# Kernel optimization log

Measured on AMD Instinct MI355X. Metric: run time of the kernel, lower is better.

The kernel has to match this reference:

```python
import jax, jax.numpy as jnp
import numpy as np

N = 50000      # nodes
E = 600000     # edges
H = 128        # hidden_features (= in_features)
ED = 16        # edge_attr_dim
B = 256        # number of graphs in batch
L = 5          # num_layers
OUT = 128      # out_features


def _xavier(key, shape):
    fan_in, fan_out = shape
    a = float(np.sqrt(6.0 / (fan_in + fan_out)))
    return jax.random.uniform(key, shape, jnp.float32, -a, a)


def setup_inputs() -> dict:
    key = jax.random.key(0)
    ks = jax.random.split(key, 32)
    x = jax.random.normal(ks[0], (N, H), jnp.float32)
    edge_index = jax.random.randint(ks[1], (2, E), 0, N, jnp.int32)
    edge_attr = jax.random.normal(ks[2], (E, ED), jnp.float32)
    batch = jnp.sort(jax.random.randint(ks[3], (N,), 0, B, jnp.int32))
    # per-layer parameters, stacked along leading L axis (in=hidden so uniform)
    node_W = jnp.stack([_xavier(jax.random.fold_in(ks[4], i), (H, H)) for i in range(L)])
    edge_W = jnp.stack([_xavier(jax.random.fold_in(ks[5], i), (ED, H)) for i in range(L)])
    mlp1_W = jnp.stack([_xavier(jax.random.fold_in(ks[6], i), (H, H)) for i in range(L)])
    mlp2_W = jnp.stack([_xavier(jax.random.fold_in(ks[7], i), (H, H)) for i in range(L)])
    zb = jnp.zeros((L, H), jnp.float32)
    # virtual-node update MLP (shared across layers) and final classifier
    vn_w0 = _xavier(ks[8], (H, H)); vn_b0 = jnp.zeros((H,), jnp.float32)
    vn_w1 = _xavier(ks[9], (H, H)); vn_b1 = jnp.zeros((H,), jnp.float32)
    fc_W = _xavier(ks[10], (H, OUT)); fc_b = jnp.zeros((OUT,), jnp.float32)
    vn_init = jnp.zeros((1, H), jnp.float32)  # embedding initialized to 0
    return {
        "x": x, "edge_attr": edge_attr,
        "node_W": node_W, "node_b": zb, "edge_W": edge_W, "edge_b": zb,
        "mlp1_W": mlp1_W, "mlp1_b": zb, "mlp2_W": mlp2_W, "mlp2_b": zb,
        "vn_w0": vn_w0, "vn_b0": vn_b0, "vn_w1": vn_w1, "vn_b1": vn_b1,
        "fc_W": fc_W, "fc_b": fc_b, "vn_init": vn_init,
        "edge_index": edge_index, "batch": batch,
    }


def reference(x, edge_attr, node_W, node_b, edge_W, edge_b, mlp1_W, mlp1_b,
              mlp2_W, mlp2_b, vn_w0, vn_b0, vn_w1, vn_b1, fc_W, fc_b,
              vn_init, edge_index, batch):
    src, dst = edge_index[0], edge_index[1]
    # per-graph node counts for mean pooling (guard against empty graphs)
    counts = jnp.maximum(
        jax.ops.segment_sum(jnp.ones((N, 1), x.dtype), batch, num_segments=B), 1.0)
    vn = jnp.broadcast_to(vn_init, (B, H))  # weight.repeat(batch_size, 1)

    def layer(carry, p):
        xc, vn = carry
        nW, nb, eW, eb, m1W, m1b, m2W, m2b = p
        h = xc @ nW + nb + vn[batch]              # node encode + VN broadcast
        ea = edge_attr @ eW + eb                   # edge encode [E,H]
        msg = h[src] + ea                          # gather + add
        agg = jax.ops.segment_sum(msg, dst, num_segments=N)  # scatter-add
        out = jax.nn.relu(agg @ m1W + m1b) @ m2W + m2b        # layer MLP
        xn = jax.nn.relu(out)
        pooled = jax.ops.segment_sum(xn, batch, num_segments=B) / counts
        vn2 = vn + jax.nn.relu(jax.nn.relu(pooled @ vn_w0 + vn_b0) @ vn_w1 + vn_b1)
        return (xn, vn2), None

    (xf, _), _ = jax.lax.scan(
        layer, (x, vn),
        (node_W, node_b, edge_W, edge_b, mlp1_W, mlp1_b, mlp2_W, mlp2_b))
    pooled = jax.ops.segment_sum(xf, batch, num_segments=B) / counts
    return pooled @ fc_W + fc_b
```

## Files before the change

### kernel.cpp

```cpp
#include <hip/hip_runtime.h>

#define NN 50000
#define EE 600000
#define HH 128
#define EDD 16
#define BB 256
#define LL 5
#define NN16 (NN * 16)
#define NSHADOW 8
#define GN 782

typedef float f32x4 __attribute__((ext_vector_type(4)));
typedef _Float16 f16x4 __attribute__((ext_vector_type(4)));
typedef _Float16 f16x8 __attribute__((ext_vector_type(8)));

__global__ __launch_bounds__(256) void wprep_all_k(
    const float* __restrict__ W0, const float* __restrict__ W1, const float* __restrict__ W2,
    _Float16* __restrict__ H0, _Float16* __restrict__ L0,
    _Float16* __restrict__ H1, _Float16* __restrict__ L1,
    _Float16* __restrict__ H2, _Float16* __restrict__ L2,
    const float* __restrict__ eW, const float* __restrict__ eb, const float* __restrict__ nb,
    _Float16* __restrict__ BXh, _Float16* __restrict__ BXl)
{
    int idx = blockIdx.x * 256 + threadIdx.x;
    if (idx < 3 * 81920) {
        int seg = idx / 81920, r = idx - seg * 81920;
        const float* W = (seg == 0) ? W0 : (seg == 1) ? W1 : W2;
        _Float16* Wh = (seg == 0) ? H0 : (seg == 1) ? H1 : H2;
        _Float16* Wl = (seg == 0) ? L0 : (seg == 1) ? L1 : L2;
        int mat = r >> 14;
        int rr = r & 16383;
        int j = rr & 7, lane = (rr >> 3) & 63, ks = (rr >> 9) & 3, ntw = (rr >> 11) & 7;
        int lm = lane & 15, quad = lane >> 4;
        int n = (ntw >> 1) * 32 + (ntw & 1) * 16 + lm;
        int k = ks * 32 + quad * 8 + j;
        float w = W[(mat << 14) + (k << 7) + n];
        _Float16 h = (_Float16)w;
        Wh[r] = h;
        Wl[r] = (_Float16)(w - (float)h);
    } else {
        int i2 = idx - 3 * 81920;
        if (i2 >= 5 * 8192) return;
        int j = i2 & 7, lane = (i2 >> 3) & 63, ks = (i2 >> 9) & 1, ntw = (i2 >> 10) & 7, l = i2 >> 13;
        int lm = lane & 15, quad = lane >> 4;
        int n = (ntw >> 1) * 32 + (ntw & 1) * 16 + lm;
        int k = ks * 32 + quad * 8 + j;
        float v = 0.f;
        if (k < 16) v = eW[((size_t)l * 16 + k) * 128 + n];
        else if (k < 32) v = eW[((size_t)l * 16 + (k - 16)) * 128 + n];
        else if (k == 32) v = eb[l * 128 + n] + nb[l * 128 + n];
        _Float16 h = (_Float16)v;
        BXh[i2] = h;
        BXl[i2] = (_Float16)(v - (float)h);
    }
}

__global__ __launch_bounds__(256) void misc_k(const float* __restrict__ x, _Float16* __restrict__ X0,
    const float* __restrict__ vninit, float* __restrict__ vn, _Float16* __restrict__ vnB,
    float* __restrict__ pooled8)
{
    int i = blockIdx.x * 256 + threadIdx.x;
    if (i < NN * 32) {
        float4 v = ((const float4*)x)[i];
        f16x4 o;
        o[0] = (_Float16)v.x; o[1] = (_Float16)v.y; o[2] = (_Float16)v.z; o[3] = (_Float16)v.w;
        ((f16x4*)X0)[i] = o;
    } else {
        int k = i - NN * 32;
        if (k < NSHADOW * BB * HH) pooled8[k] = 0.f;
        if (k < BB * HH) { vn[k] = vninit[k & 127]; vnB[k] = (_Float16)0; }
    }
}

__device__ __forceinline__ void mfma_stage16(
    const _Float16* __restrict__ As,
    const _Float16* __restrict__ Wh, const _Float16* __restrict__ Wl,
    int wn, int lm, int quad, int lane, f32x4 acc[4][2])
{
    f16x8 Bh[2][4], Bl[2][4];
#pragma unroll
    for (int nt = 0; nt < 2; ++nt)
#pragma unroll
        for (int ks = 0; ks < 4; ++ks) {
            int fi = ((((wn * 2 + nt) * 4) + ks) * 64 + lane) * 8;
            Bh[nt][ks] = *(const f16x8*)(Wh + fi);
            Bl[nt][ks] = *(const f16x8*)(Wl + fi);
        }
#pragma unroll
    for (int ks = 0; ks < 4; ++ks) {
        f16x8 a[4];
#pragma unroll
        for (int mt = 0; mt < 4; ++mt) {
            int off = (mt * 16 + lm) * 136 + ks * 32 + quad * 8;
            a[mt] = *(const f16x8*)(As + off);
        }
#pragma unroll
        for (int mt = 0; mt < 4; ++mt)
#pragma unroll
            for (int nt = 0; nt < 2; ++nt) {
                acc[mt][nt] = __builtin_amdgcn_mfma_f32_16x16x32_f16(a[mt], Bh[nt][ks], acc[mt][nt], 0, 0, 0);
                acc[mt][nt] = __builtin_amdgcn_mfma_f32_16x16x32_f16(a[mt], Bl[nt][ks], acc[mt][nt], 0, 0, 0);
            }
    }
}

__device__ __forceinline__ void store_f16(const _Float16* __restrict__ Fo,
    _Float16* __restrict__ out, int M, int brow, int tid)
{
    const int r = tid >> 2, cg = tid & 3;
    const int grow = brow + r;
    if (grow >= M) return;
    const f16x8* src = (const f16x8*)(Fo + r * 136 + cg * 32);
    f16x8* dst = (f16x8*)(out + (size_t)grow * 128 + cg * 32);
#pragma unroll
    for (int i = 0; i < 4; ++i) dst[i] = src[i];
}

__global__ __launch_bounds__(256) void layer_k(
    const _Float16* __restrict__ Xin,
    const _Float16* __restrict__ Afix,
    const _Float16* __restrict__ Cfrag, const _Float16* __restrict__ vnB, int usevn,
    const int* __restrict__ rowstart, const int2* __restrict__ csr,
    const _Float16* __restrict__ WNh, const _Float16* __restrict__ WNl,
    const _Float16* __restrict__ BXh, const _Float16* __restrict__ BXl,
    const _Float16* __restrict__ W1h, const _Float16* __restrict__ W1l, const float* __restrict__ b1,
    const _Float16* __restrict__ W2h, const _Float16* __restrict__ W2l, const float* __restrict__ b2,
    _Float16* __restrict__ Xout, float* __restrict__ pooled8,
    const int* __restrict__ batch, int M)
{
    __shared__ __align__(16) _Float16 bufA[64 * 136];
    __shared__ __align__(16) _Float16 bufB[64 * 136];
    const int tid = threadIdx.x, brow = blockIdx.x * 64;

    {
        const int r = tid >> 2, cg = tid & 3;
        const int grow = brow + r;
        _Float16* p = bufB + r * 72 + cg * 16;
        if (grow < M) {
            const f16x8* s = (const f16x8*)(Afix + (size_t)grow * 64 + cg * 16);
            ((f16x8*)p)[0] = s[0]; ((f16x8*)p)[1] = s[1];
        } else {
            f16x8 z = (f16x8)(_Float16)0;
            ((f16x8*)p)[0] = z; ((f16x8*)p)[1] = z;
        }
    }

    {
        const int wv = tid >> 6, grp = (tid >> 4) & 3, li = tid & 15;
        const f16x8* X8 = (const f16x8*)Xin;
        for (int j = 0; j < 4; ++j) {
            int rnode = wv * 16 + grp * 4 + j;
            int node = brow + rnode;
            f16x8 o = (f16x8)(_Float16)0;
            if (node < M) {
                int s = rowstart[node], e = rowstart[node + 1];
                float ax[8];
#pragma unroll
                for (int k = 0; k < 8; ++k) ax[k] = 0.f;
                int p = s;
                for (; p + 4 <= e; p += 4) {
                    int s0 = csr[p].x, s1 = csr[p + 1].x, s2 = csr[p + 2].x, s3 = csr[p + 3].x;
                    f16x8 x0 = X8[(size_t)s0 * 16 + li];
                    f16x8 x1 = X8[(size_t)s1 * 16 + li];
                    f16x8 x2 = X8[(size_t)s2 * 16 + li];
                    f16x8 x3 = X8[(size_t)s3 * 16 + li];
#pragma unroll
                    for (int k = 0; k < 8; ++k)
                        ax[k] += ((float)x0[k] + (float)x1[k]) + ((float)x2[k] + (float)x3[k]);
                }
                for (; p < e; ++p) {
                    f16x8 x0 = X8[(size_t)csr[p].x * 16 + li];
#pragma unroll
                    for (int k = 0; k < 8; ++k) ax[k] += (float)x0[k];
                }
#pragma unroll
                for (int k = 0; k < 8; ++k) o[k] = (_Float16)ax[k];
            }
            *(f16x8*)(bufA + rnode * 136 + li * 8) = o;
        }
    }
    __syncthreads();

    const int lane = tid & 63, wn = tid >> 6, lm = lane & 15, quad = lane >> 4;
    const int colb = wn * 32 + lm;

    f32x4 acc[4][2];
#pragma unroll
    for (int mt = 0; mt < 4; ++mt) { acc[mt][0] = (f32x4)(0.f); acc[mt][1] = (f32x4)(0.f); }

    mfma_stage16(bufA, WNh, WNl, wn, lm, quad, lane, acc);

#pragma unroll
    for (int ksf = 0; ksf < 2; ++ksf) {
        f16x8 Bh[2], Bl[2];
#pragma unroll
        for (int nt = 0; nt < 2; ++nt) {
            int fi = (((wn * 2 + nt) * 2 + ksf) * 64 + lane) * 8;
            Bh[nt] = *(const f16x8*)(BXh + fi);
            Bl[nt] = *(const f16x8*)(BXl + fi);
        }
#pragma unroll
        for (int mt = 0; mt < 4; ++mt) {
            f16x8 a = *(const f16x8*)(bufB + (mt * 16 + lm) * 72 + ksf * 32 + quad * 8);
#pragma unroll
            for (int nt = 0; nt < 2; ++nt) {
                acc[mt][nt] = __builtin_amdgcn_mfma_f32_16x16x32_f16(a, Bh[nt], acc[mt][nt], 0, 0, 0);
                acc[mt][nt] = __builtin_amdgcn_mfma_f32_16x16x32_f16(a, Bl[nt], acc[mt][nt], 0, 0, 0);
            }
        }
    }

    if (usevn) {
        const _Float16* Cb = Cfrag + (size_t)blockIdx.x * 16384;
#pragma unroll
        for (int ks = 0; ks < 8; ++ks) {
            f16x8 bv[2];
#pragma unroll
            for (int nt = 0; nt < 2; ++nt)
                bv[nt] = *(const f16x8*)(vnB + (((ks * 8 + (wn * 2 + nt)) * 64 + lane) * 8));
#pragma unroll
            for (int mt = 0; mt < 4; ++mt) {
                f16x8 av = *(const f16x8*)(Cb + (((mt * 8 + ks) * 64 + lane) * 8));
                acc[mt][0] = __builtin_amdgcn_mfma_f32_16x16x32_f16(av, bv[0], acc[mt][0], 0, 0, 0);
                acc[mt][1] = __builtin_amdgcn_mfma_f32_16x16x32_f16(av, bv[1], acc[mt][1], 0, 0, 0);
            }
        }
    }
    __syncthreads();

#pragma unroll
    for (int mt = 0; mt < 4; ++mt) {
#pragma unroll
        for (int r = 0; r < 4; ++r) {
            int trow = mt * 16 + quad * 4 + r;
            bufA[trow * 136 + colb]      = (_Float16)acc[mt][0][r];
            bufA[trow * 136 + colb + 16] = (_Float16)acc[mt][1][r];
        }
    }
    __syncthreads();

#pragma unroll
    for (int mt = 0; mt < 4; ++mt) { acc[mt][0] = (f32x4)(0.f); acc[mt][1] = (f32x4)(0.f); }
    mfma_stage16(bufA, W1h, W1l, wn, lm, quad, lane, acc);
    {
        const float c0 = b1[colb], c1 = b1[colb + 16];
#pragma unroll
        for (int mt = 0; mt < 4; ++mt) {
#pragma unroll
            for (int r = 0; r < 4; ++r) {
                int trow = mt * 16 + quad * 4 + r;
                bufB[trow * 136 + colb]      = (_Float16)fmaxf(acc[mt][0][r] + c0, 0.f);
                bufB[trow * 136 + colb + 16] = (_Float16)fmaxf(acc[mt][1][r] + c1, 0.f);
            }
        }
    }
    __syncthreads();

#pragma unroll
    for (int mt = 0; mt < 4; ++mt) { acc[mt][0] = (f32x4)(0.f); acc[mt][1] = (f32x4)(0.f); }
    mfma_stage16(bufB, W2h, W2l, wn, lm, quad, lane, acc);
    {
        const float d0 = b2[colb], d1 = b2[colb + 16];
#pragma unroll
        for (int mt = 0; mt < 4; ++mt) {
#pragma unroll
            for (int r = 0; r < 4; ++r) {
                int trow = mt * 16 + quad * 4 + r;
                bufA[trow * 136 + colb]      = (_Float16)fmaxf(acc[mt][0][r] + d0, 0.f);
                bufA[trow * 136 + colb + 16] = (_Float16)fmaxf(acc[mt][1][r] + d1, 0.f);
            }
        }
    }
    __syncthreads();
    store_f16(bufA, Xout, M, brow, tid);

    {
        float* pooled = pooled8 + (size_t)(blockIdx.x & (NSHADOW - 1)) * (BB * HH);
        const int c = tid & 127, half = tid >> 7;
        const int row0 = half * 32;
        float sum = 0.f;
        int curg = -1;
        for (int r2 = 0; r2 < 32; ++r2) {
            int grow = brow + row0 + r2;
            if (grow >= M) break;
            int g = batch[grow];
            if (g != curg) {
                if (curg >= 0) atomicAdd(&pooled[curg * 128 + c], sum);
                curg = g; sum = 0.f;
            }
            sum += (float)bufA[(row0 + r2) * 136 + c];
        }
        if (curg >= 0) atomicAdd(&pooled[curg * 128 + c], sum);
    }
}

__global__ __launch_bounds__(256) void aggfix_k(
    const float* __restrict__ eattr, const int* __restrict__ rowstart,
    const int2* __restrict__ csr, _Float16* __restrict__ Afix, int n)
{
    const int lane = threadIdx.x & 15;
    const int node = blockIdx.x * 16 + (threadIdx.x >> 4);
    if (node >= n) return;
    const int s = rowstart[node], e = rowstart[node + 1];
    float acc = 0.f;
    for (int p = s; p < e; ++p)
        acc += eattr[(size_t)csr[p].y * 16 + lane];
    _Float16 hi = (_Float16)acc;
    _Float16 lo = (_Float16)(acc - (float)hi);
    _Float16* A = Afix + (size_t)node * 64;
    A[lane] = hi;
    A[16 + lane] = lo;
    A[32 + lane] = (lane == 0) ? (_Float16)(float)(e - s) : (_Float16)0;
    A[48 + lane] = (_Float16)0;
}

__global__ void histboth_k(const int* __restrict__ dstv, const int* __restrict__ srcv,
                           const int* __restrict__ batch,
                           int* __restrict__ degp, unsigned int* __restrict__ Cpack)
{
    int i = blockIdx.x * 256 + threadIdx.x;
    if (i >= EE) return;
    int d = dstv[i];
    atomicAdd(&degp[(blockIdx.x & 3) * NN16 + (d << 4)], 1);
    int g = batch[srcv[i]];
    int blk = d >> 6, rib = d & 63, mt = rib >> 4, lm = rib & 15;
    int ks = g >> 5, quad = (g >> 3) & 3, j = g & 7;
    size_t e = (size_t)blk * 16384 + (size_t)(((mt * 8 + ks) * 64) + quad * 16 + lm) * 8 + j;
    atomicAdd(&Cpack[e >> 1], 1u << ((e & 1) * 16));
}

__global__ __launch_bounds__(256) void ccvt_k(unsigned int* __restrict__ Cpack)
{
    int i = blockIdx.x * 256 + threadIdx.x;
    if (i >= GN * 16384 / 2) return;
    unsigned int v = Cpack[i];
    _Float16 lo = (_Float16)(float)(v & 0xffffu);
    _Float16 hi = (_Float16)(float)(v >> 16);
    unsigned short lu = __builtin_bit_cast(unsigned short, lo);
    unsigned short hu = __builtin_bit_cast(unsigned short, hi);
    Cpack[i] = (unsigned int)lu | ((unsigned int)hu << 16);
}

__global__ __launch_bounds__(128) void vn_update_k(
    float* __restrict__ pooled8, const int* __restrict__ gstart,
    const float* __restrict__ W0, const float* __restrict__ b0,
    const float* __restrict__ W1, const float* __restrict__ b1,
    float* __restrict__ vn, _Float16* __restrict__ vnB)
{
    __shared__ float p[128], q[128];
    const int g = blockIdx.x, t = threadIdx.x;
    float cnt = (float)(gstart[g + 1] - gstart[g]);
    if (cnt < 1.f) cnt = 1.f;
    float sum = 0.f;
#pragma unroll
    for (int s = 0; s < NSHADOW; ++s) {
        float* slot = pooled8 + (size_t)s * (BB * HH) + g * 128 + t;
        sum += *slot;
        *slot = 0.f;
    }
    p[t] = sum / cnt;
    __syncthreads();
    float a0 = b0[t];
    for (int k = 0; k < 128; ++k) a0 = fmaf(p[k], W0[k * 128 + t], a0);
    q[t] = fmaxf(a0, 0.f);
    __syncthreads();
    float a1 = b1[t];
    for (int k = 0; k < 128; ++k) a1 = fmaf(q[k], W1[k * 128 + t], a1);
    float nv = vn[g * 128 + t] + fmaxf(a1, 0.f);
    vn[g * 128 + t] = nv;
    {
        int ks = g >> 5, quad = (g >> 3) & 3, j = g & 7;
        int tt = ((t >> 5) << 1) | ((t >> 4) & 1);
        int lanev = quad * 16 + (t & 15);
        vnB[((ks * 8 + tt) * 64 + lanev) * 8 + j] = (_Float16)nv;
    }
}

__global__ __launch_bounds__(128) void fc_k(
    const float* __restrict__ pooled8, const int* __restrict__ gstart,
    const float* __restrict__ W, const float* __restrict__ b,
    float* __restrict__ out)
{
    __shared__ float p[128];
    const int g = blockIdx.x, t = threadIdx.x;
    float cnt = (float)(gstart[g + 1] - gstart[g]);
    if (cnt < 1.f) cnt = 1.f;
    float sum = 0.f;
#pragma unroll
    for (int s = 0; s < NSHADOW; ++s)
        sum += pooled8[(size_t)s * (BB * HH) + g * 128 + t];
    p[t] = sum / cnt;
    __syncthreads();
    float acc = b[t];
    for (int k = 0; k < 128; ++k) acc = fmaf(p[k], W[k * 128 + t], acc);
    out[g * 128 + t] = acc;
}

__global__ void scan_deg_k(const int* __restrict__ degp, int n, int* __restrict__ out, int* __restrict__ bsum)
{
    __shared__ int s[256];
    int gid = blockIdx.x * 256 + threadIdx.x;
    int v = 0;
    if (gid < n) {
        int o = gid << 4;
        v = degp[o] + degp[NN16 + o] + degp[2 * NN16 + o] + degp[3 * NN16 + o];
    }
    s[threadIdx.x] = v;
    __syncthreads();
    for (int off = 1; off < 256; off <<= 1) {
        int t = (threadIdx.x >= off) ? s[threadIdx.x - off] : 0;
        __syncthreads();
        s[threadIdx.x] += t;
        __syncthreads();
    }
    int incl = s[threadIdx.x];
    if (gid < n) out[gid] = incl - v;
    if (bsum != nullptr && threadIdx.x == 255) bsum[blockIdx.x] = incl;
}

__global__ void scan_k(const int* __restrict__ in, int n, int* __restrict__ out,
                       const int* __restrict__ batch, int* __restrict__ gstart)
{
    __shared__ int s[256];
    int v = (threadIdx.x < n) ? in[threadIdx.x] : 0;
    s[threadIdx.x] = v;
    __syncthreads();
    for (int off = 1; off < 256; off <<= 1) {
        int t = (threadIdx.x >= off) ? s[threadIdx.x - off] : 0;
        __syncthreads();
        s[threadIdx.x] += t;
        __syncthreads();
    }
    if (threadIdx.x < n) out[threadIdx.x] = s[threadIdx.x] - v;
    {
        int b = threadIdx.x;
        int lo = 0, hi = NN;
        while (lo < hi) {
            int mid = (lo + hi) >> 1;
            if (batch[mid] < b) lo = mid + 1; else hi = mid;
        }
        gstart[b] = lo;
        if (threadIdx.x == 0) gstart[BB] = NN;
    }
}

__global__ void addoff_k(int* __restrict__ data, const int* __restrict__ boff,
                         int* __restrict__ cursorp, int n, int total)
{
    int i = blockIdx.x * 256 + threadIdx.x;
    if (i < n) {
        int v = data[i] + boff[blockIdx.x];
        data[i] = v;
        cursorp[i << 4] = v;
    }
    if (i == 0) data[n] = total;
}

__global__ void fill_k(const int* __restrict__ dst, const int* __restrict__ src, int n,
                       int* __restrict__ cursorp, int2* __restrict__ csr)
{
    int e = blockIdx.x * 256 + threadIdx.x;
    if (e < n) {
        int slot = atomicAdd(&cursorp[dst[e] << 4], 1);
        int2 pr; pr.x = src[e]; pr.y = e;
        csr[slot] = pr;
    }
}

extern "C" void kernel_launch(void* const* d_in, const int* in_sizes, int n_in,
                              void* d_out, int out_size, void* d_ws, size_t ws_size,
                              hipStream_t stream)
{
    (void)in_sizes; (void)n_in; (void)out_size; (void)ws_size;
    const float* x       = (const float*)d_in[0];
    const float* eattr   = (const float*)d_in[1];
    const float* node_W  = (const float*)d_in[2];
    const float* node_b  = (const float*)d_in[3];
    const float* edge_W  = (const float*)d_in[4];
    const float* edge_b  = (const float*)d_in[5];
    const float* mlp1_W  = (const float*)d_in[6];
    const float* mlp1_b  = (const float*)d_in[7];
    const float* mlp2_W  = (const float*)d_in[8];
    const float* mlp2_b  = (const float*)d_in[9];
    const float* vn_w0   = (const float*)d_in[10];
    const float* vn_b0   = (const float*)d_in[11];
    const float* vn_w1   = (const float*)d_in[12];
    const float* vn_b1   = (const float*)d_in[13];
    const float* fc_W    = (const float*)d_in[14];
    const float* fc_b    = (const float*)d_in[15];
    const float* vn_init = (const float*)d_in[16];
    const int*   eidx    = (const int*)d_in[17];
    const int*   batch   = (const int*)d_in[18];
    const int* srcv = eidx;
    const int* dstv = eidx + EE;

    char* wp = (char*)d_ws;
    auto alloc = [&](size_t bytes) -> void* {
        void* p = (void*)wp;
        wp += (bytes + 255) & ~(size_t)255;
        return p;
    };
    int* degp       = (int*)alloc((size_t)4 * NN16 * 4);
    _Float16* Cfrag = (_Float16*)alloc((size_t)GN * 16384 * 2);
    const size_t zero_bytes = (size_t)4 * NN16 * 4 + (size_t)GN * 16384 * 2;

    _Float16* X0   = (_Float16*)alloc((size_t)NN * HH * 2);
    _Float16* X1   = (_Float16*)alloc((size_t)NN * HH * 2);
    _Float16* X2   = (_Float16*)alloc((size_t)NN * HH * 2);
    _Float16* Afix = (_Float16*)alloc((size_t)NN * 64 * 2);
    float* vn      = (float*)alloc((size_t)BB * HH * 4);
    _Float16* vnB  = (_Float16*)alloc((size_t)BB * HH * 2);
    float* pooled8 = (float*)alloc((size_t)NSHADOW * BB * HH * 4);
    int* rowstart  = (int*)alloc((size_t)(NN + 1) * 4);
    int* cursorp   = (int*)alloc((size_t)NN16 * 4);
    int2* csr      = (int2*)alloc((size_t)EE * 8);
    int* bsum      = (int*)alloc(256 * 4);
    int* boff      = (int*)alloc(256 * 4);
    int* gstart    = (int*)alloc((size_t)(BB + 1) * 4);
    _Float16* WtN_h = (_Float16*)alloc((size_t)5 * 16384 * 2);
    _Float16* WtN_l = (_Float16*)alloc((size_t)5 * 16384 * 2);
    _Float16* Wt1_h = (_Float16*)alloc((size_t)5 * 16384 * 2);
    _Float16* Wt1_l = (_Float16*)alloc((size_t)5 * 16384 * 2);
    _Float16* Wt2_h = (_Float16*)alloc((size_t)5 * 16384 * 2);
    _Float16* Wt2_l = (_Float16*)alloc((size_t)5 * 16384 * 2);
    _Float16* BXh   = (_Float16*)alloc((size_t)5 * 8192 * 2);
    _Float16* BXl   = (_Float16*)alloc((size_t)5 * 8192 * 2);

    (void)hipMemsetAsync(degp, 0, zero_bytes, stream);

    histboth_k<<<(EE + 255) / 256, 256, 0, stream>>>(dstv, srcv, batch, degp, (unsigned int*)Cfrag);

    const int NB1 = (NN + 255) / 256;
    scan_deg_k<<<NB1, 256, 0, stream>>>(degp, NN, rowstart, bsum);
    scan_k<<<1, 256, 0, stream>>>(bsum, NB1, boff, batch, gstart);
    addoff_k<<<NB1, 256, 0, stream>>>(rowstart, boff, cursorp, NN, EE);
    fill_k<<<(EE + 255) / 256, 256, 0, stream>>>(dstv, srcv, EE, cursorp, csr);
    aggfix_k<<<(NN + 15) / 16, 256, 0, stream>>>(eattr, rowstart, csr, Afix, NN);
    ccvt_k<<<(GN * 16384 / 2 + 255) / 256, 256, 0, stream>>>((unsigned int*)Cfrag);

    misc_k<<<(NN * 32 + NSHADOW * BB * HH) / 256, 256, 0, stream>>>(x, X0, vn_init, vn, vnB, pooled8);
    wprep_all_k<<<(3 * 81920 + 5 * 8192) / 256, 256, 0, stream>>>(
        node_W, mlp1_W, mlp2_W, WtN_h, WtN_l, Wt1_h, Wt1_l, Wt2_h, Wt2_l,
        edge_W, edge_b, node_b, BXh, BXl);

    const _Float16* xin = X0;
    for (int l = 0; l < LL; ++l) {
        _Float16* xout = (l & 1) ? X2 : X1;
        layer_k<<<GN, 256, 0, stream>>>(xin, Afix, Cfrag, vnB, (l > 0) ? 1 : 0,
            rowstart, csr,
            WtN_h + (size_t)l * 16384, WtN_l + (size_t)l * 16384,
            BXh + (size_t)l * 8192, BXl + (size_t)l * 8192,
            Wt1_h + (size_t)l * 16384, Wt1_l + (size_t)l * 16384, mlp1_b + (size_t)l * HH,
            Wt2_h + (size_t)l * 16384, Wt2_l + (size_t)l * 16384, mlp2_b + (size_t)l * HH,
            xout, pooled8, batch, NN);
        if (l < LL - 1)
            vn_update_k<<<BB, 128, 0, stream>>>(pooled8, gstart, vn_w0, vn_b0, vn_w1, vn_b1, vn, vnB);
        xin = xout;
    }
    fc_k<<<BB, 128, 0, stream>>>(pooled8, gstart, fc_W, fc_b, (float*)d_out);
}
```

Before: 558.6 us.

## Drop second LDS buffer, split CSR arrays, interleave two-node gathers in layer kernel

The layer kernel drops its second shared-memory tile and reuses one buffer, adding barriers between stages. The Afix edge-attribute fragment is now read directly from global memory, and its allocation is padded to whole blocks and zeroed. The CSR array is split into separate source and edge-id arrays so the gather reads only 4-byte source indices. The neighbour gather processes two nodes at once to keep more loads in flight. Halving LDS use per block aims to raise occupancy; the cost is extra syncs, higher register pressure from the doubled accumulators, and uncoalesced global fragment loads.

```diff
diff --git a/kernel.cpp b/kernel.cpp
--- a/kernel.cpp
+++ b/kernel.cpp
@@ -120,7 +120,7 @@
     const _Float16* __restrict__ Xin,
     const _Float16* __restrict__ Afix,
     const _Float16* __restrict__ Cfrag, const _Float16* __restrict__ vnB, int usevn,
-    const int* __restrict__ rowstart, const int2* __restrict__ csr,
+    const int* __restrict__ rowstart, const int* __restrict__ csrc,
     const _Float16* __restrict__ WNh, const _Float16* __restrict__ WNl,
     const _Float16* __restrict__ BXh, const _Float16* __restrict__ BXl,
     const _Float16* __restrict__ W1h, const _Float16* __restrict__ W1l, const float* __restrict__ b1,
@@ -129,54 +129,76 @@
     const int* __restrict__ batch, int M)
 {
     __shared__ __align__(16) _Float16 bufA[64 * 136];
-    __shared__ __align__(16) _Float16 bufB[64 * 136];
     const int tid = threadIdx.x, brow = blockIdx.x * 64;
-
-    {
-        const int r = tid >> 2, cg = tid & 3;
-        const int grow = brow + r;
-        _Float16* p = bufB + r * 72 + cg * 16;
-        if (grow < M) {
-            const f16x8* s = (const f16x8*)(Afix + (size_t)grow * 64 + cg * 16);
-            ((f16x8*)p)[0] = s[0]; ((f16x8*)p)[1] = s[1];
-        } else {
-            f16x8 z = (f16x8)(_Float16)0;
-            ((f16x8*)p)[0] = z; ((f16x8*)p)[1] = z;
-        }
-    }
 
     {
         const int wv = tid >> 6, grp = (tid >> 4) & 3, li = tid & 15;
         const f16x8* X8 = (const f16x8*)Xin;
-        for (int j = 0; j < 4; ++j) {
-            int rnode = wv * 16 + grp * 4 + j;
-            int node = brow + rnode;
-            f16x8 o = (f16x8)(_Float16)0;
-            if (node < M) {
-                int s = rowstart[node], e = rowstart[node + 1];
-                float ax[8];
-#pragma unroll
-                for (int k = 0; k < 8; ++k) ax[k] = 0.f;
-                int p = s;
-                for (; p + 4 <= e; p += 4) {
-                    int s0 = csr[p].x, s1 = csr[p + 1].x, s2 = csr[p + 2].x, s3 = csr[p + 3].x;
-                    f16x8 x0 = X8[(size_t)s0 * 16 + li];
-                    f16x8 x1 = X8[(size_t)s1 * 16 + li];
-                    f16x8 x2 = X8[(size_t)s2 * 16 + li];
-                    f16x8 x3 = X8[(size_t)s3 * 16 + li];
-#pragma unroll
-                    for (int k = 0; k < 8; ++k)
-                        ax[k] += ((float)x0[k] + (float)x1[k]) + ((float)x2[k] + (float)x3[k]);
+#pragma unroll
+        for (int jj = 0; jj < 2; ++jj) {
+            int rn0 = wv * 16 + grp * 4 + jj * 2;
+            int rn1 = rn0 + 1;
+            int n0 = brow + rn0, n1 = brow + rn1;
+            int s0 = 0, e0 = 0, s1 = 0, e1 = 0;
+            if (n0 < M) { s0 = rowstart[n0]; e0 = rowstart[n0 + 1]; }
+            if (n1 < M) { s1 = rowstart[n1]; e1 = rowstart[n1 + 1]; }
+            float ax0[8], ax1[8];
+#pragma unroll
+            for (int k = 0; k < 8; ++k) { ax0[k] = 0.f; ax1[k] = 0.f; }
+            int p0 = s0, p1 = s1;
+            while (p0 + 4 <= e0 && p1 + 4 <= e1) {
+                int a0 = csrc[p0], a1 = csrc[p0 + 1], a2 = csrc[p0 + 2], a3 = csrc[p0 + 3];
+                int b0 = csrc[p1], b1v = csrc[p1 + 1], b2v = csrc[p1 + 2], b3 = csrc[p1 + 3];
+                f16x8 xa0 = X8[(size_t)a0 * 16 + li];
+                f16x8 xa1 = X8[(size_t)a1 * 16 + li];
+                f16x8 xa2 = X8[(size_t)a2 * 16 + li];
+                f16x8 xa3 = X8[(size_t)a3 * 16 + li];
+                f16x8 xb0 = X8[(size_t)b0 * 16 + li];
+                f16x8 xb1 = X8[(size_t)b1v * 16 + li];
+                f16x8 xb2 = X8[(size_t)b2v * 16 + li];
+                f16x8 xb3 = X8[(size_t)b3 * 16 + li];
+#pragma unroll
+                for (int k = 0; k < 8; ++k) {
+                    ax0[k] += ((float)xa0[k] + (float)xa1[k]) + ((float)xa2[k] + (float)xa3[k]);
+                    ax1[k] += ((float)xb0[k] + (float)xb1[k]) + ((float)xb2[k] + (float)xb3[k]);
                 }
-                for (; p < e; ++p) {
-                    f16x8 x0 = X8[(size_t)csr[p].x * 16 + li];
-#pragma unroll
-                    for (int k = 0; k < 8; ++k) ax[k] += (float)x0[k];
-                }
-#pragma unroll
-                for (int k = 0; k < 8; ++k) o[k] = (_Float16)ax[k];
-            }
-            *(f16x8*)(bufA + rnode * 136 + li * 8) = o;
+                p0 += 4; p1 += 4;
+            }
+            for (; p0 + 4 <= e0; p0 += 4) {
+                int a0 = csrc[p0], a1 = csrc[p0 + 1], a2 = csrc[p0 + 2], a3 = csrc[p0 + 3];
+                f16x8 xa0 = X8[(size_t)a0 * 16 + li];
+                f16x8 xa1 = X8[(size_t)a1 * 16 + li];
+                f16x8 xa2 = X8[(size_t)a2 * 16 + li];
+                f16x8 xa3 = X8[(size_t)a3 * 16 + li];
+#pragma unroll
+                for (int k = 0; k < 8; ++k)
+                    ax0[k] += ((float)xa0[k] + (float)xa1[k]) + ((float)xa2[k] + (float)xa3[k]);
+            }
+            for (; p1 + 4 <= e1; p1 += 4) {
+                int b0 = csrc[p1], b1v = csrc[p1 + 1], b2v = csrc[p1 + 2], b3 = csrc[p1 + 3];
+                f16x8 xb0 = X8[(size_t)b0 * 16 + li];
+                f16x8 xb1 = X8[(size_t)b1v * 16 + li];
+                f16x8 xb2 = X8[(size_t)b2v * 16 + li];
+                f16x8 xb3 = X8[(size_t)b3 * 16 + li];
+#pragma unroll
+                for (int k = 0; k < 8; ++k)
+                    ax1[k] += ((float)xb0[k] + (float)xb1[k]) + ((float)xb2[k] + (float)xb3[k]);
+            }
+            for (; p0 < e0; ++p0) {
+                f16x8 x0 = X8[(size_t)csrc[p0] * 16 + li];
+#pragma unroll
+                for (int k = 0; k < 8; ++k) ax0[k] += (float)x0[k];
+            }
+            for (; p1 < e1; ++p1) {
+                f16x8 x0 = X8[(size_t)csrc[p1] * 16 + li];
+#pragma unroll
+                for (int k = 0; k < 8; ++k) ax1[k] += (float)x0[k];
+            }
+            f16x8 o0, o1;
+#pragma unroll
+            for (int k = 0; k < 8; ++k) { o0[k] = (_Float16)ax0[k]; o1[k] = (_Float16)ax1[k]; }
+            *(f16x8*)(bufA + rn0 * 136 + li * 8) = o0;
+            *(f16x8*)(bufA + rn1 * 136 + li * 8) = o1;
         }
     }
     __syncthreads();
@@ -187,8 +209,6 @@
     f32x4 acc[4][2];
 #pragma unroll
     for (int mt = 0; mt < 4; ++mt) { acc[mt][0] = (f32x4)(0.f); acc[mt][1] = (f32x4)(0.f); }
-
-    mfma_stage16(bufA, WNh, WNl, wn, lm, quad, lane, acc);
 
 #pragma unroll
     for (int ksf = 0; ksf < 2; ++ksf) {
@@ -201,7 +221,7 @@
         }
 #pragma unroll
         for (int mt = 0; mt < 4; ++mt) {
-            f16x8 a = *(const f16x8*)(bufB + (mt * 16 + lm) * 72 + ksf * 32 + quad * 8);
+            f16x8 a = *(const f16x8*)(Afix + (size_t)(brow + mt * 16 + lm) * 64 + ksf * 32 + quad * 8);
 #pragma unroll
             for (int nt = 0; nt < 2; ++nt) {
                 acc[mt][nt] = __builtin_amdgcn_mfma_f32_16x16x32_f16(a, Bh[nt], acc[mt][nt], 0, 0, 0);
@@ -226,6 +246,8 @@
             }
         }
     }
+
+    mfma_stage16(bufA, WNh, WNl, wn, lm, quad, lane, acc);
     __syncthreads();
 
 #pragma unroll
@@ -242,6 +264,7 @@
 #pragma unroll
     for (int mt = 0; mt < 4; ++mt) { acc[mt][0] = (f32x4)(0.f); acc[mt][1] = (f32x4)(0.f); }
     mfma_stage16(bufA, W1h, W1l, wn, lm, quad, lane, acc);
+    __syncthreads();
     {
         const float c0 = b1[colb], c1 = b1[colb + 16];
 #pragma unroll
@@ -249,8 +272,8 @@
 #pragma unroll
             for (int r = 0; r < 4; ++r) {
                 int trow = mt * 16 + quad * 4 + r;
-                bufB[trow * 136 + colb]      = (_Float16)fmaxf(acc[mt][0][r] + c0, 0.f);
-                bufB[trow * 136 + colb + 16] = (_Float16)fmaxf(acc[mt][1][r] + c1, 0.f);
+                bufA[trow * 136 + colb]      = (_Float16)fmaxf(acc[mt][0][r] + c0, 0.f);
+                bufA[trow * 136 + colb + 16] = (_Float16)fmaxf(acc[mt][1][r] + c1, 0.f);
             }
         }
     }
@@ -258,7 +281,8 @@
 
 #pragma unroll
     for (int mt = 0; mt < 4; ++mt) { acc[mt][0] = (f32x4)(0.f); acc[mt][1] = (f32x4)(0.f); }
-    mfma_stage16(bufB, W2h, W2l, wn, lm, quad, lane, acc);
+    mfma_stage16(bufA, W2h, W2l, wn, lm, quad, lane, acc);
+    __syncthreads();
     {
         const float d0 = b2[colb], d1 = b2[colb + 16];
 #pragma unroll
@@ -296,7 +320,7 @@
 
 __global__ __launch_bounds__(256) void aggfix_k(
     const float* __restrict__ eattr, const int* __restrict__ rowstart,
-    const int2* __restrict__ csr, _Float16* __restrict__ Afix, int n)
+    const int* __restrict__ cedge, _Float16* __restrict__ Afix, int n)
 {
     const int lane = threadIdx.x & 15;
     const int node = blockIdx.x * 16 + (threadIdx.x >> 4);
@@ -304,7 +328,7 @@
     const int s = rowstart[node], e = rowstart[node + 1];
     float acc = 0.f;
     for (int p = s; p < e; ++p)
-        acc += eattr[(size_t)csr[p].y * 16 + lane];
+        acc += eattr[(size_t)cedge[p] * 16 + lane];
     _Float16 hi = (_Float16)acc;
     _Float16 lo = (_Float16)(acc - (float)hi);
     _Float16* A = Afix + (size_t)node * 64;
@@ -457,13 +481,13 @@
 }
 
 __global__ void fill_k(const int* __restrict__ dst, const int* __restrict__ src, int n,
-                       int* __restrict__ cursorp, int2* __restrict__ csr)
+                       int* __restrict__ cursorp, int* __restrict__ csrc, int* __restrict__ cedge)
 {
     int e = blockIdx.x * 256 + threadIdx.x;
     if (e < n) {
         int slot = atomicAdd(&cursorp[dst[e] << 4], 1);
-        int2 pr; pr.x = src[e]; pr.y = e;
-        csr[slot] = pr;
+        csrc[slot] = src[e];
+        cedge[slot] = e;
     }
 }
 
@@ -502,18 +526,19 @@
     };
     int* degp       = (int*)alloc((size_t)4 * NN16 * 4);
     _Float16* Cfrag = (_Float16*)alloc((size_t)GN * 16384 * 2);
-    const size_t zero_bytes = (size_t)4 * NN16 * 4 + (size_t)GN * 16384 * 2;
+    _Float16* Afix  = (_Float16*)alloc((size_t)GN * 64 * 64 * 2);
+    const size_t zero_bytes = (size_t)4 * NN16 * 4 + (size_t)GN * 16384 * 2 + (size_t)GN * 64 * 64 * 2;
 
     _Float16* X0   = (_Float16*)alloc((size_t)NN * HH * 2);
     _Float16* X1   = (_Float16*)alloc((size_t)NN * HH * 2);
     _Float16* X2   = (_Float16*)alloc((size_t)NN * HH * 2);
-    _Float16* Afix = (_Float16*)alloc((size_t)NN * 64 * 2);
     float* vn      = (float*)alloc((size_t)BB * HH * 4);
     _Float16* vnB  = (_Float16*)alloc((size_t)BB * HH * 2);
     float* pooled8 = (float*)alloc((size_t)NSHADOW * BB * HH * 4);
     int* rowstart  = (int*)alloc((size_t)(NN + 1) * 4);
     int* cursorp   = (int*)alloc((size_t)NN16 * 4);
-    int2* csr      = (int2*)alloc((size_t)EE * 8);
+    int* csrc      = (int*)alloc((size_t)EE * 4);
+    int* cedge     = (int*)alloc((size_t)EE * 4);
     int* bsum      = (int*)alloc(256 * 4);
     int* boff      = (int*)alloc(256 * 4);
     int* gstart    = (int*)alloc((size_t)(BB + 1) * 4);
@@ -534,8 +559,8 @@
     scan_deg_k<<<NB1, 256, 0, stream>>>(degp, NN, rowstart, bsum);
     scan_k<<<1, 256, 0, stream>>>(bsum, NB1, boff, batch, gstart);
     addoff_k<<<NB1, 256, 0, stream>>>(rowstart, boff, cursorp, NN, EE);
-    fill_k<<<(EE + 255) / 256, 256, 0, stream>>>(dstv, srcv, EE, cursorp, csr);
-    aggfix_k<<<(NN + 15) / 16, 256, 0, stream>>>(eattr, rowstart, csr, Afix, NN);
+    fill_k<<<(EE + 255) / 256, 256, 0, stream>>>(dstv, srcv, EE, cursorp, csrc, cedge);
+    aggfix_k<<<(NN + 15) / 16, 256, 0, stream>>>(eattr, rowstart, cedge, Afix, NN);
     ccvt_k<<<(GN * 16384 / 2 + 255) / 256, 256, 0, stream>>>((unsigned int*)Cfrag);
 
     misc_k<<<(NN * 32 + NSHADOW * BB * HH) / 256, 256, 0, stream>>>(x, X0, vn_init, vn, vnB, pooled8);
@@ -547,7 +572,7 @@
     for (int l = 0; l < LL; ++l) {
         _Float16* xout = (l & 1) ? X2 : X1;
         layer_k<<<GN, 256, 0, stream>>>(xin, Afix, Cfrag, vnB, (l > 0) ? 1 : 0,
-            rowstart, csr,
+            rowstart, csrc,
             WtN_h + (size_t)l * 16384, WtN_l + (size_t)l * 16384,
             BXh + (size_t)l * 8192, BXl + (size_t)l * 8192,
             Wt1_h + (size_t)l * 16384, Wt1_l + (size_t)l * 16384, mlp1_b + (size_t)l * HH,
```

After: 682.2 us. 22.1% more time.

## Gather virtual-node rows per edge instead of dense count-matrix MFMA

Applied to the files above, without the earlier changes.

Replaces the per-block graph-count matrix (Cfrag) times vn MFMA with a direct per-edge gather of the source graph's fp16 virtual-node row, summed alongside the neighbor features. The CSR entry is packed so the source node and its graph id share one 32-bit word, and edge ids move to a separate array. This drops the count histogram atomics, the conversion kernel and 8 MFMA k-steps per block. In exchange it adds an extra gather per edge in layers 1-4 and reads Afix fragments straight from global memory. Packing the source node into 16 bits with a 0xffff mask cannot represent node ids above 65535; N is 50000 here, so it fits.

```diff
diff --git a/kernel.cpp b/kernel.cpp
--- a/kernel.cpp
+++ b/kernel.cpp
@@ -56,7 +56,7 @@
 }
 
 __global__ __launch_bounds__(256) void misc_k(const float* __restrict__ x, _Float16* __restrict__ X0,
-    const float* __restrict__ vninit, float* __restrict__ vn, _Float16* __restrict__ vnB,
+    const float* __restrict__ vninit, float* __restrict__ vn, _Float16* __restrict__ vn16,
     float* __restrict__ pooled8)
 {
     int i = blockIdx.x * 256 + threadIdx.x;
@@ -68,7 +68,7 @@
     } else {
         int k = i - NN * 32;
         if (k < NSHADOW * BB * HH) pooled8[k] = 0.f;
-        if (k < BB * HH) { vn[k] = vninit[k & 127]; vnB[k] = (_Float16)0; }
+        if (k < BB * HH) { vn[k] = vninit[k & 127]; vn16[k] = (_Float16)0; }
     }
 }
 
@@ -119,8 +119,8 @@
 __global__ __launch_bounds__(256) void layer_k(
     const _Float16* __restrict__ Xin,
     const _Float16* __restrict__ Afix,
-    const _Float16* __restrict__ Cfrag, const _Float16* __restrict__ vnB, int usevn,
-    const int* __restrict__ rowstart, const int2* __restrict__ csr,
+    const _Float16* __restrict__ vn16, int usevn,
+    const int* __restrict__ rowstart, const unsigned int* __restrict__ csrc,
     const _Float16* __restrict__ WNh, const _Float16* __restrict__ WNl,
     const _Float16* __restrict__ BXh, const _Float16* __restrict__ BXl,
     const _Float16* __restrict__ W1h, const _Float16* __restrict__ W1l, const float* __restrict__ b1,
@@ -133,50 +133,55 @@
     const int tid = threadIdx.x, brow = blockIdx.x * 64;
 
     {
-        const int r = tid >> 2, cg = tid & 3;
-        const int grow = brow + r;
-        _Float16* p = bufB + r * 72 + cg * 16;
-        if (grow < M) {
-            const f16x8* s = (const f16x8*)(Afix + (size_t)grow * 64 + cg * 16);
-            ((f16x8*)p)[0] = s[0]; ((f16x8*)p)[1] = s[1];
-        } else {
-            f16x8 z = (f16x8)(_Float16)0;
-            ((f16x8*)p)[0] = z; ((f16x8*)p)[1] = z;
-        }
-    }
-
-    {
         const int wv = tid >> 6, grp = (tid >> 4) & 3, li = tid & 15;
         const f16x8* X8 = (const f16x8*)Xin;
+        const f16x8* V8 = (const f16x8*)vn16;
         for (int j = 0; j < 4; ++j) {
             int rnode = wv * 16 + grp * 4 + j;
             int node = brow + rnode;
             f16x8 o = (f16x8)(_Float16)0;
+            f16x8 ov = (f16x8)(_Float16)0;
             if (node < M) {
                 int s = rowstart[node], e = rowstart[node + 1];
-                float ax[8];
-#pragma unroll
-                for (int k = 0; k < 8; ++k) ax[k] = 0.f;
+                float ax[8], ev[8];
+#pragma unroll
+                for (int k = 0; k < 8; ++k) { ax[k] = 0.f; ev[k] = 0.f; }
                 int p = s;
                 for (; p + 4 <= e; p += 4) {
-                    int s0 = csr[p].x, s1 = csr[p + 1].x, s2 = csr[p + 2].x, s3 = csr[p + 3].x;
-                    f16x8 x0 = X8[(size_t)s0 * 16 + li];
-                    f16x8 x1 = X8[(size_t)s1 * 16 + li];
-                    f16x8 x2 = X8[(size_t)s2 * 16 + li];
-                    f16x8 x3 = X8[(size_t)s3 * 16 + li];
+                    unsigned c0 = csrc[p], c1 = csrc[p + 1], c2 = csrc[p + 2], c3 = csrc[p + 3];
+                    f16x8 x0 = X8[(size_t)(c0 & 0xffffu) * 16 + li];
+                    f16x8 x1 = X8[(size_t)(c1 & 0xffffu) * 16 + li];
+                    f16x8 x2 = X8[(size_t)(c2 & 0xffffu) * 16 + li];
+                    f16x8 x3 = X8[(size_t)(c3 & 0xffffu) * 16 + li];
 #pragma unroll
                     for (int k = 0; k < 8; ++k)
                         ax[k] += ((float)x0[k] + (float)x1[k]) + ((float)x2[k] + (float)x3[k]);
+                    if (usevn) {
+                        f16x8 v0 = V8[(c0 >> 16) * 16 + li];
+                        f16x8 v1 = V8[(c1 >> 16) * 16 + li];
+                        f16x8 v2 = V8[(c2 >> 16) * 16 + li];
+                        f16x8 v3 = V8[(c3 >> 16) * 16 + li];
+#pragma unroll
+                        for (int k = 0; k < 8; ++k)
+                            ev[k] += ((float)v0[k] + (float)v1[k]) + ((float)v2[k] + (float)v3[k]);
+                    }
                 }
                 for (; p < e; ++p) {
-                    f16x8 x0 = X8[(size_t)csr[p].x * 16 + li];
+                    unsigned c0 = csrc[p];
+                    f16x8 x0 = X8[(size_t)(c0 & 0xffffu) * 16 + li];
 #pragma unroll
                     for (int k = 0; k < 8; ++k) ax[k] += (float)x0[k];
+                    if (usevn) {
+                        f16x8 v0 = V8[(c0 >> 16) * 16 + li];
+#pragma unroll
+                        for (int k = 0; k < 8; ++k) ev[k] += (float)v0[k];
+                    }
                 }
 #pragma unroll
-                for (int k = 0; k < 8; ++k) o[k] = (_Float16)ax[k];
+                for (int k = 0; k < 8; ++k) { o[k] = (_Float16)ax[k]; ov[k] = (_Float16)ev[k]; }
             }
             *(f16x8*)(bufA + rnode * 136 + li * 8) = o;
+            *(f16x8*)(bufB + rnode * 136 + li * 8) = ov;
         }
     }
     __syncthreads();
@@ -187,8 +192,6 @@
     f32x4 acc[4][2];
 #pragma unroll
     for (int mt = 0; mt < 4; ++mt) { acc[mt][0] = (f32x4)(0.f); acc[mt][1] = (f32x4)(0.f); }
-
-    mfma_stage16(bufA, WNh, WNl, wn, lm, quad, lane, acc);
 
 #pragma unroll
     for (int ksf = 0; ksf < 2; ++ksf) {
@@ -201,7 +204,7 @@
         }
 #pragma unroll
         for (int mt = 0; mt < 4; ++mt) {
-            f16x8 a = *(const f16x8*)(bufB + (mt * 16 + lm) * 72 + ksf * 32 + quad * 8);
+            f16x8 a = *(const f16x8*)(Afix + (size_t)(brow + mt * 16 + lm) * 64 + ksf * 32 + quad * 8);
 #pragma unroll
             for (int nt = 0; nt < 2; ++nt) {
                 acc[mt][nt] = __builtin_amdgcn_mfma_f32_16x16x32_f16(a, Bh[nt], acc[mt][nt], 0, 0, 0);
@@ -210,22 +213,7 @@
         }
     }
 
-    if (usevn) {
-        const _Float16* Cb = Cfrag + (size_t)blockIdx.x * 16384;
-#pragma unroll
-        for (int ks = 0; ks < 8; ++ks) {
-            f16x8 bv[2];
-#pragma unroll
-            for (int nt = 0; nt < 2; ++nt)
-                bv[nt] = *(const f16x8*)(vnB + (((ks * 8 + (wn * 2 + nt)) * 64 + lane) * 8));
-#pragma unroll
-            for (int mt = 0; mt < 4; ++mt) {
-                f16x8 av = *(const f16x8*)(Cb + (((mt * 8 + ks) * 64 + lane) * 8));
-                acc[mt][0] = __builtin_amdgcn_mfma_f32_16x16x32_f16(av, bv[0], acc[mt][0], 0, 0, 0);
-                acc[mt][1] = __builtin_amdgcn_mfma_f32_16x16x32_f16(av, bv[1], acc[mt][1], 0, 0, 0);
-            }
-        }
-    }
+    mfma_stage16(bufA, WNh, WNl, wn, lm, quad, lane, acc);
     __syncthreads();
 
 #pragma unroll
@@ -233,8 +221,8 @@
 #pragma unroll
         for (int r = 0; r < 4; ++r) {
             int trow = mt * 16 + quad * 4 + r;
-            bufA[trow * 136 + colb]      = (_Float16)acc[mt][0][r];
-            bufA[trow * 136 + colb + 16] = (_Float16)acc[mt][1][r];
+            bufA[trow * 136 + colb]      = (_Float16)(acc[mt][0][r] + (float)bufB[trow * 136 + colb]);
+            bufA[trow * 136 + colb + 16] = (_Float16)(acc[mt][1][r] + (float)bufB[trow * 136 + colb + 16]);
         }
     }
     __syncthreads();
@@ -296,7 +284,7 @@
 
 __global__ __launch_bounds__(256) void aggfix_k(
     const float* __restrict__ eattr, const int* __restrict__ rowstart,
-    const int2* __restrict__ csr, _Float16* __restrict__ Afix, int n)
+    const int* __restrict__ cedge, _Float16* __restrict__ Afix, int n)
 {
     const int lane = threadIdx.x & 15;
     const int node = blockIdx.x * 16 + (threadIdx.x >> 4);
@@ -304,7 +292,7 @@
     const int s = rowstart[node], e = rowstart[node + 1];
     float acc = 0.f;
     for (int p = s; p < e; ++p)
-        acc += eattr[(size_t)csr[p].y * 16 + lane];
+        acc += eattr[(size_t)cedge[p] * 16 + lane];
     _Float16 hi = (_Float16)acc;
     _Float16 lo = (_Float16)(acc - (float)hi);
     _Float16* A = Afix + (size_t)node * 64;
@@ -314,38 +302,17 @@
     A[48 + lane] = (_Float16)0;
 }
 
-__global__ void histboth_k(const int* __restrict__ dstv, const int* __restrict__ srcv,
-                           const int* __restrict__ batch,
-                           int* __restrict__ degp, unsigned int* __restrict__ Cpack)
+__global__ void histp_k(const int* __restrict__ idx, int n, int* __restrict__ cntp)
 {
     int i = blockIdx.x * 256 + threadIdx.x;
-    if (i >= EE) return;
-    int d = dstv[i];
-    atomicAdd(&degp[(blockIdx.x & 3) * NN16 + (d << 4)], 1);
-    int g = batch[srcv[i]];
-    int blk = d >> 6, rib = d & 63, mt = rib >> 4, lm = rib & 15;
-    int ks = g >> 5, quad = (g >> 3) & 3, j = g & 7;
-    size_t e = (size_t)blk * 16384 + (size_t)(((mt * 8 + ks) * 64) + quad * 16 + lm) * 8 + j;
-    atomicAdd(&Cpack[e >> 1], 1u << ((e & 1) * 16));
-}
-
-__global__ __launch_bounds__(256) void ccvt_k(unsigned int* __restrict__ Cpack)
-{
-    int i = blockIdx.x * 256 + threadIdx.x;
-    if (i >= GN * 16384 / 2) return;
-    unsigned int v = Cpack[i];
-    _Float16 lo = (_Float16)(float)(v & 0xffffu);
-    _Float16 hi = (_Float16)(float)(v >> 16);
-    unsigned short lu = __builtin_bit_cast(unsigned short, lo);
-    unsigned short hu = __builtin_bit_cast(unsigned short, hi);
-    Cpack[i] = (unsigned int)lu | ((unsigned int)hu << 16);
+    if (i < n) atomicAdd(&cntp[(blockIdx.x & 3) * NN16 + (idx[i] << 4)], 1);
 }
 
 __global__ __launch_bounds__(128) void vn_update_k(
     float* __restrict__ pooled8, const int* __restrict__ gstart,
     const float* __restrict__ W0, const float* __restrict__ b0,
     const float* __restrict__ W1, const float* __restrict__ b1,
-    float* __restrict__ vn, _Float16* __restrict__ vnB)
+    float* __restrict__ vn, _Float16* __restrict__ vn16)
 {
     __shared__ float p[128], q[128];
     const int g = blockIdx.x, t = threadIdx.x;
@@ -368,12 +335,7 @@
     for (int k = 0; k < 128; ++k) a1 = fmaf(q[k], W1[k * 128 + t], a1);
     float nv = vn[g * 128 + t] + fmaxf(a1, 0.f);
     vn[g * 128 + t] = nv;
-    {
-        int ks = g >> 5, quad = (g >> 3) & 3, j = g & 7;
-        int tt = ((t >> 5) << 1) | ((t >> 4) & 1);
-        int lanev = quad * 16 + (t & 15);
-        vnB[((ks * 8 + tt) * 64 + lanev) * 8 + j] = (_Float16)nv;
-    }
+    vn16[g * 128 + t] = (_Float16)nv;
 }
 
 __global__ __launch_bounds__(128) void fc_k(
@@ -457,13 +419,17 @@
 }
 
 __global__ void fill_k(const int* __restrict__ dst, const int* __restrict__ src, int n,
-                       int* __restrict__ cursorp, int2* __restrict__ csr)
+                       const int* __restrict__ batch,
+                       int* __restrict__ cursorp, unsigned int* __restrict__ csrc,
+                       int* __restrict__ cedge)
 {
     int e = blockIdx.x * 256 + threadIdx.x;
     if (e < n) {
+        int sv = src[e];
+        unsigned g = (unsigned)batch[sv];
         int slot = atomicAdd(&cursorp[dst[e] << 4], 1);
-        int2 pr; pr.x = src[e]; pr.y = e;
-        csr[slot] = pr;
+        csrc[slot] = (unsigned)sv | (g << 16);
+        cedge[slot] = e;
     }
 }
 
@@ -501,19 +467,19 @@
         return p;
     };
     int* degp       = (int*)alloc((size_t)4 * NN16 * 4);
-    _Float16* Cfrag = (_Float16*)alloc((size_t)GN * 16384 * 2);
-    const size_t zero_bytes = (size_t)4 * NN16 * 4 + (size_t)GN * 16384 * 2;
+    _Float16* Afix  = (_Float16*)alloc((size_t)GN * 64 * 64 * 2);
+    const size_t zero_bytes = (size_t)4 * NN16 * 4 + (size_t)GN * 64 * 64 * 2;
 
     _Float16* X0   = (_Float16*)alloc((size_t)NN * HH * 2);
     _Float16* X1   = (_Float16*)alloc((size_t)NN * HH * 2);
     _Float16* X2   = (_Float16*)alloc((size_t)NN * HH * 2);
-    _Float16* Afix = (_Float16*)alloc((size_t)NN * 64 * 2);
     float* vn      = (float*)alloc((size_t)BB * HH * 4);
-    _Float16* vnB  = (_Float16*)alloc((size_t)BB * HH * 2);
+    _Float16* vn16 = (_Float16*)alloc((size_t)BB * HH * 2);
     float* pooled8 = (float*)alloc((size_t)NSHADOW * BB * HH * 4);
     int* rowstart  = (int*)alloc((size_t)(NN + 1) * 4);
     int* cursorp   = (int*)alloc((size_t)NN16 * 4);
-    int2* csr      = (int2*)alloc((size_t)EE * 8);
+    unsigned int* csrc = (unsigned int*)alloc((size_t)EE * 4);
+    int* cedge     = (int*)alloc((size_t)EE * 4);
     int* bsum      = (int*)alloc(256 * 4);
     int* boff      = (int*)alloc(256 * 4);
     int* gstart    = (int*)alloc((size_t)(BB + 1) * 4);
@@ -528,17 +494,16 @@
 
     (void)hipMemsetAsync(degp, 0, zero_bytes, stream);
 
-    histboth_k<<<(EE + 255) / 256, 256, 0, stream>>>(dstv, srcv, batch, degp, (unsigned int*)Cfrag);
+    histp_k<<<(EE + 255) / 256, 256, 0, stream>>>(dstv, EE, degp);
 
     const int NB1 = (NN + 255) / 256;
     scan_deg_k<<<NB1, 256, 0, stream>>>(degp, NN, rowstart, bsum);
     scan_k<<<1, 256, 0, stream>>>(bsum, NB1, boff, batch, gstart);
     addoff_k<<<NB1, 256, 0, stream>>>(rowstart, boff, cursorp, NN, EE);
-    fill_k<<<(EE + 255) / 256, 256, 0, stream>>>(dstv, srcv, EE, cursorp, csr);
-    aggfix_k<<<(NN + 15) / 16, 256, 0, stream>>>(eattr, rowstart, csr, Afix, NN);
-    ccvt_k<<<(GN * 16384 / 2 + 255) / 256, 256, 0, stream>>>((unsigned int*)Cfrag);
-
-    misc_k<<<(NN * 32 + NSHADOW * BB * HH) / 256, 256, 0, stream>>>(x, X0, vn_init, vn, vnB, pooled8);
+    fill_k<<<(EE + 255) / 256, 256, 0, stream>>>(dstv, srcv, EE, batch, cursorp, csrc, cedge);
+    aggfix_k<<<(NN + 15) / 16, 256, 0, stream>>>(eattr, rowstart, cedge, Afix, NN);
+
+    misc_k<<<(NN * 32 + NSHADOW * BB * HH) / 256, 256, 0, stream>>>(x, X0, vn_init, vn, vn16, pooled8);
     wprep_all_k<<<(3 * 81920 + 5 * 8192) / 256, 256, 0, stream>>>(
         node_W, mlp1_W, mlp2_W, WtN_h, WtN_l, Wt1_h, Wt1_l, Wt2_h, Wt2_l,
         edge_W, edge_b, node_b, BXh, BXl);
@@ -546,15 +511,15 @@
     const _Float16* xin = X0;
     for (int l = 0; l < LL; ++l) {
         _Float16* xout = (l & 1) ? X2 : X1;
-        layer_k<<<GN, 256, 0, stream>>>(xin, Afix, Cfrag, vnB, (l > 0) ? 1 : 0,
-            rowstart, csr,
+        layer_k<<<GN, 256, 0, stream>>>(xin, Afix, vn16, (l > 0) ? 1 : 0,
+            rowstart, csrc,
             WtN_h + (size_t)l * 16384, WtN_l + (size_t)l * 16384,
             BXh + (size_t)l * 8192, BXl + (size_t)l * 8192,
             Wt1_h + (size_t)l * 16384, Wt1_l + (size_t)l * 16384, mlp1_b + (size_t)l * HH,
             Wt2_h + (size_t)l * 16384, Wt2_l + (size_t)l * 16384, mlp2_b + (size_t)l * HH,
             xout, pooled8, batch, NN);
         if (l < LL - 1)
-            vn_update_k<<<BB, 128, 0, stream>>>(pooled8, gstart, vn_w0, vn_b0, vn_w1, vn_b1, vn, vnB);
+            vn_update_k<<<BB, 128, 0, stream>>>(pooled8, gstart, vn_w0, vn_b0, vn_w1, vn_b1, vn, vn16);
         xin = xout;
     }
     fc_k<<<BB, 128, 0, stream>>>(pooled8, gstart, fc_W, fc_b, (float*)d_out);
```

Result: slower. 655.4 us (+17.3%).
